# Performance work log

Measured on AMD Instinct MI355X. Metric: run time of the kernel, lower is better.

The kernel has to match this reference:

```python
import jax, jax.numpy as jnp
import numpy as np
import math

HIDDEN = 2048
NUM_HEADS = 32
NUM_KV_HEADS = 8
HEAD_DIM = HIDDEN // NUM_HEADS
GROUPS = NUM_HEADS // NUM_KV_HEADS
B, S = 2, 2048


def setup_inputs() -> dict:
    key = jax.random.key(0)
    ks = jax.random.split(key, 9)
    sc = 1.0 / math.sqrt(HIDDEN)
    x = jax.random.normal(ks[0], (B, S, HIDDEN), dtype=jnp.float32)
    # causal mask: 1 where attention allowed, 0 where masked
    mask = jnp.tril(jnp.ones((S, S), dtype=jnp.int32))[None, None, :, :]
    Wq = jax.random.normal(ks[1], (HIDDEN, HIDDEN), dtype=jnp.float32) * sc
    bq = jnp.zeros((HIDDEN,), dtype=jnp.float32)
    Wk = jax.random.normal(ks[2], (NUM_KV_HEADS * HEAD_DIM, HIDDEN), dtype=jnp.float32) * sc
    bk = jnp.zeros((NUM_KV_HEADS * HEAD_DIM,), dtype=jnp.float32)
    Wv = jax.random.normal(ks[3], (NUM_KV_HEADS * HEAD_DIM, HIDDEN), dtype=jnp.float32) * sc
    bv = jnp.zeros((NUM_KV_HEADS * HEAD_DIM,), dtype=jnp.float32)
    Wo = jax.random.normal(ks[4], (HIDDEN, HIDDEN), dtype=jnp.float32) * sc
    bo = jnp.zeros((HIDDEN,), dtype=jnp.float32)
    return {"x": x, "mask": mask, "Wq": Wq, "bq": bq, "Wk": Wk, "bk": bk,
            "Wv": Wv, "bv": bv, "Wo": Wo, "bo": bo}


def reference(x, mask, Wq, bq, Wk, bk, Wv, bv, Wo, bo):
    b, s, _ = x.shape
    # projections (torch Linear: y = x @ W.T + b)
    Q = (x @ Wq.T + bq).reshape(b, s, NUM_HEADS, HEAD_DIM).transpose(0, 2, 1, 3)  # b h s d
    K = (x @ Wk.T + bk).reshape(b, s, NUM_KV_HEADS, HEAD_DIM).transpose(0, 2, 1, 3)
    V = (x @ Wv.T + bv).reshape(b, s, NUM_KV_HEADS, HEAD_DIM).transpose(0, 2, 1, 3)
    # repeat_kv expansion
    K = jnp.repeat(K, GROUPS, axis=1)  # b h s d
    V = jnp.repeat(V, GROUPS, axis=1)
    scores = jnp.einsum('bhqd,bhkd->bhqk', Q, K) / math.sqrt(HEAD_DIM)
    scores = jnp.where(mask == 0, jnp.float32(-jnp.inf), scores)
    w = jax.nn.softmax(scores, axis=-1)
    # dropout is identity in eval mode
    out = jnp.einsum('bhqk,bhkd->bhqd', w, V)
    out = out.transpose(0, 2, 1, 3).reshape(b, s, HIDDEN)
    return out @ Wo.T + bo
```

## Files before the change

kernel.cpp:

```cpp
#include <hip/hip_runtime.h>
#include <hip/hip_bf16.h>
#include <stdint.h>

#define HID   2048
#define SLEN  2048
#define NB    2
#define NHEADS 32
#define NKVH   8
#define HDIM   64
#define KVW    512

typedef __bf16 bf16_t;
typedef __bf16 bf16x4 __attribute__((ext_vector_type(4)));
typedef __bf16 bf16x8 __attribute__((ext_vector_type(8)));
typedef float  f32x4  __attribute__((ext_vector_type(4)));

__device__ __forceinline__ f32x4 mfma16(bf16x8 a, bf16x8 b, f32x4 c) {
  return __builtin_amdgcn_mfma_f32_16x16x32_bf16(a, b, c, 0, 0, 0);
}

__device__ __forceinline__ void gl2lds16(const bf16_t* g, bf16_t* l) {
  __builtin_amdgcn_global_load_lds(
      (const __attribute__((address_space(1))) void*)g,
      (__attribute__((address_space(3))) void*)l,
      16, 0, 0);
}

__device__ __forceinline__ float fast_exp2(float x) {
#if __has_builtin(__builtin_amdgcn_exp2f)
  return __builtin_amdgcn_exp2f(x);
#else
  return __expf(x * 0.69314718f);
#endif
}

__device__ __forceinline__ bf16x8 ld8(const bf16_t* p) {
  return *(const bf16x8*)p;
}
__device__ __forceinline__ bf16x8 ld8(const float* p) {
  f32x4 a = *(const f32x4*)p;
  f32x4 b = *(const f32x4*)(p + 4);
  bf16x8 r;
  r[0] = (bf16_t)a[0]; r[1] = (bf16_t)a[1]; r[2] = (bf16_t)a[2]; r[3] = (bf16_t)a[3];
  r[4] = (bf16_t)b[0]; r[5] = (bf16_t)b[1]; r[6] = (bf16_t)b[2]; r[7] = (bf16_t)b[3];
  return r;
}

__device__ __forceinline__ void st_c(bf16_t* p, float v) { *p = (bf16_t)v; }
__device__ __forceinline__ void st_c(float*  p, float v) { *p = v; }

__global__ __launch_bounds__(256) void cvt_kernel(
    const float* __restrict__ x,  const float* __restrict__ wq,
    const float* __restrict__ wk, const float* __restrict__ wv,
    const float* __restrict__ wo,
    bf16_t* xb, bf16_t* wqb, bf16_t* wkb, bf16_t* wvb, bf16_t* wob)
{
  const float* s; bf16_t* d; size_t n;
  switch (blockIdx.y) {
    case 0:  s = x;  d = xb;  n = (size_t)NB * SLEN * HID; break;
    case 1:  s = wq; d = wqb; n = (size_t)HID * HID; break;
    case 2:  s = wk; d = wkb; n = (size_t)KVW * HID; break;
    case 3:  s = wv; d = wvb; n = (size_t)KVW * HID; break;
    default: s = wo; d = wob; n = (size_t)HID * HID; break;
  }
  const size_t stride = (size_t)gridDim.x * 256 * 8;
  for (size_t i = ((size_t)blockIdx.x * 256 + threadIdx.x) * 8; i < n; i += stride)
    *(bf16x8*)(d + i) = ld8(s + i);
}

template <typename CT, bool TRANSV>
__device__ __forceinline__ void gemm128_dma(
    const bf16_t* __restrict__ Ap, int lda,
    const bf16_t* __restrict__ Wp, int ldw,
    const float* __restrict__ biasp,
    CT* __restrict__ Cp, int ldc, int K,
    bf16_t* __restrict__ Al, bf16_t* __restrict__ Bl)
{
  const int tid  = threadIdx.x;
  const int lane = tid & 63;
  const int w    = tid >> 6;
  const int fr   = lane & 15;
  const int quad = lane >> 4;
  const int wm   = (w >> 1) * 64;
  const int wn   = (w & 1) * 64;

  const f32x4 z4 = {0.f, 0.f, 0.f, 0.f};
  f32x4 acc[4][4];
  for (int i = 0; i < 4; ++i)
    for (int j = 0; j < 4; ++j) acc[i][j] = z4;

  const int c0   = w * 4;
  const int srow = lane >> 2;
  const int skc  = (lane & 3) * 8;

  for (int k0 = 0; k0 < K; k0 += 64) {
    for (int t = 0; t < 4; ++t) {
      const int c  = c0 + t;
      const int r  = (c & 7) * 16 + srow;
      const int kk = k0 + (c >> 3) * 32 + skc;
      gl2lds16(Ap + (size_t)r * lda + kk, &Al[c * 512 + lane * 8]);
      gl2lds16(Wp + (size_t)r * ldw + kk, &Bl[c * 512 + lane * 8]);
    }
    __syncthreads();
    for (int ks = 0; ks < 2; ++ks) {
      bf16x8 af[4], bfr[4];
      for (int mi = 0; mi < 4; ++mi)
        af[mi] = *(const bf16x8*)&Al[ks * 4096 + (wm + mi * 16 + fr) * 32 + quad * 8];
      for (int ni = 0; ni < 4; ++ni)
        bfr[ni] = *(const bf16x8*)&Bl[ks * 4096 + (wn + ni * 16 + fr) * 32 + quad * 8];
      for (int mi = 0; mi < 4; ++mi)
        for (int ni = 0; ni < 4; ++ni)
          acc[mi][ni] = mfma16(af[mi], bfr[ni], acc[mi][ni]);
    }
    __syncthreads();
  }

  for (int ni = 0; ni < 4; ++ni) {
    const int col = wn + ni * 16 + fr;
    const float bz = biasp[col];
    for (int mi = 0; mi < 4; ++mi) {
      const int r0 = wm + mi * 16 + quad * 4;
      if constexpr (TRANSV) {
        bf16x4 pk;
        for (int r = 0; r < 4; ++r) pk[r] = (bf16_t)(acc[mi][ni][r] + bz);
        *(bf16x4*)&Cp[(size_t)col * ldc + r0] = pk;
      } else {
        for (int r = 0; r < 4; ++r)
          st_c(Cp + (size_t)(r0 + r) * ldc + col, acc[mi][ni][r] + bz);
      }
    }
  }
}

__global__ __launch_bounds__(256) void qkv_dma_kernel(
    const bf16_t* __restrict__ xb,
    const bf16_t* __restrict__ Wqb, const float* __restrict__ bq,
    const bf16_t* __restrict__ Wkb, const float* __restrict__ bk,
    const bf16_t* __restrict__ Wvb, const float* __restrict__ bv,
    bf16_t* Qb, bf16_t* Kb, bf16_t* VbT)
{
  __shared__ __align__(16) bf16_t Al[2 * 4096];
  __shared__ __align__(16) bf16_t Bl[2 * 4096];

  const int nb = blockIdx.x;
  const int mb = blockIdx.y;
  const bf16_t* A = xb + (size_t)mb * 128 * HID;
  if (nb < 16) {
    gemm128_dma<bf16_t, false>(A, HID, Wqb + (size_t)nb * 128 * HID, HID,
                               bq + nb * 128,
                               Qb + (size_t)mb * 128 * HID + nb * 128, HID, HID,
                               Al, Bl);
  } else if (nb < 20) {
    const int j = nb - 16;
    gemm128_dma<bf16_t, false>(A, HID, Wkb + (size_t)j * 128 * HID, HID,
                               bk + j * 128,
                               Kb + (size_t)mb * 128 * KVW + j * 128, KVW, HID,
                               Al, Bl);
  } else {
    const int j = nb - 20;
    const int b = mb >> 4;
    bf16_t* Cv = VbT + ((size_t)(b * NKVH + j * 2) * HDIM) * SLEN + (mb & 15) * 128;
    gemm128_dma<bf16_t, true>(A, HID, Wvb + (size_t)j * 128 * HID, HID,
                              bv + j * 128, Cv, SLEN, HID, Al, Bl);
  }
}

__global__ __launch_bounds__(256) void oproj_dma_kernel(
    const bf16_t* __restrict__ A, const bf16_t* __restrict__ Wob,
    const float* __restrict__ bo, float* out)
{
  __shared__ __align__(16) bf16_t Al[2 * 4096];
  __shared__ __align__(16) bf16_t Bl[2 * 4096];
  const int nb = blockIdx.x, mb = blockIdx.y;
  gemm128_dma<float, false>(A + (size_t)mb * 128 * HID, HID,
                            Wob + (size_t)nb * 128 * HID, HID,
                            bo + nb * 128,
                            out + (size_t)mb * 128 * HID + nb * 128, HID, HID,
                            Al, Bl);
}

template <typename AT, typename CT>
__device__ __forceinline__ void gemm128_tile(
    const AT* __restrict__ Ap, int lda,
    const float* __restrict__ Wp, int ldw,
    const float* __restrict__ biasp,
    CT* __restrict__ Cp, int ldc,
    int K)
{
  __shared__ __align__(16) bf16_t Al[128 * 32];
  __shared__ __align__(16) bf16_t Bl[128 * 32];

  const int tid  = threadIdx.x;
  const int lane = tid & 63;
  const int w    = tid >> 6;
  const int fr   = lane & 15;
  const int quad = lane >> 4;
  const int wm   = (w >> 1) * 64;
  const int wn   = (w & 1) * 64;

  const f32x4 z4 = {0.f, 0.f, 0.f, 0.f};
  f32x4 acc[4][4];
  for (int i = 0; i < 4; ++i)
    for (int j = 0; j < 4; ++j) acc[i][j] = z4;

  const int c0    = w * 2;
  const int srow0 = lane >> 2;
  const int skc   = (lane & 3) * 8;

  for (int k0 = 0; k0 < K; k0 += 32) {
    bf16x8 av[2], bv[2];
    for (int t = 0; t < 2; ++t) {
      const int r = (c0 + t) * 16 + srow0;
      av[t] = ld8(Ap + (size_t)r * lda + k0 + skc);
      bv[t] = ld8(Wp + (size_t)r * ldw + k0 + skc);
    }
    for (int t = 0; t < 2; ++t) {
      const int c = c0 + t;
      *(bf16x8*)&Al[c * 512 + lane * 8] = av[t];
      *(bf16x8*)&Bl[c * 512 + lane * 8] = bv[t];
    }
    __syncthreads();
    bf16x8 af[4], bfr[4];
    for (int mi = 0; mi < 4; ++mi)
      af[mi] = *(const bf16x8*)&Al[(wm + mi * 16 + fr) * 32 + quad * 8];
    for (int ni = 0; ni < 4; ++ni)
      bfr[ni] = *(const bf16x8*)&Bl[(wn + ni * 16 + fr) * 32 + quad * 8];
    for (int mi = 0; mi < 4; ++mi)
      for (int ni = 0; ni < 4; ++ni)
        acc[mi][ni] = mfma16(af[mi], bfr[ni], acc[mi][ni]);
    __syncthreads();
  }

  for (int ni = 0; ni < 4; ++ni) {
    const int col = wn + ni * 16 + fr;
    const float bz = biasp[col];
    for (int mi = 0; mi < 4; ++mi) {
      const int r0 = wm + mi * 16 + quad * 4;
      for (int r = 0; r < 4; ++r)
        st_c(Cp + (size_t)(r0 + r) * ldc + col, acc[mi][ni][r] + bz);
    }
  }
}

__global__ __launch_bounds__(256) void qkv_kernel(
    const float* __restrict__ x,
    const float* __restrict__ Wq, const float* __restrict__ bq,
    const float* __restrict__ Wk, const float* __restrict__ bk,
    const float* __restrict__ Wv, const float* __restrict__ bv,
    bf16_t* Qb, bf16_t* Kb, bf16_t* Vb)
{
  const int nb = blockIdx.x;
  const int mb = blockIdx.y;
  const float* W; const float* bias; bf16_t* C; int ldc;
  if (nb < 16)      { W = Wq + (size_t)nb * 128 * HID;  bias = bq + nb * 128;
                      C = Qb + nb * 128; ldc = HID; }
  else if (nb < 20) { const int j = nb - 16;
                      W = Wk + (size_t)j * 128 * HID;   bias = bk + j * 128;
                      C = Kb + j * 128; ldc = KVW; }
  else              { const int j = nb - 20;
                      W = Wv + (size_t)j * 128 * HID;   bias = bv + j * 128;
                      C = Vb + j * 128; ldc = KVW; }
  gemm128_tile<float, bf16_t>(x + (size_t)mb * 128 * HID, HID, W, HID, bias,
                              C + (size_t)mb * 128 * ldc, ldc, HID);
}

__global__ __launch_bounds__(256) void oproj_kernel(
    const bf16_t* __restrict__ A, const float* __restrict__ Wo,
    const float* __restrict__ bo, float* out)
{
  const int nb = blockIdx.x, mb = blockIdx.y;
  gemm128_tile<bf16_t, float>(A + (size_t)mb * 128 * HID, HID,
                              Wo + (size_t)nb * 128 * HID, HID,
                              bo + nb * 128,
                              out + (size_t)mb * 128 * HID + nb * 128, HID, HID);
}

__global__ __launch_bounds__(256) void vtrans_kernel(
    const bf16_t* __restrict__ Vb, bf16_t* __restrict__ VbT)
{
  __shared__ bf16_t T[64][72];
  const int st = blockIdx.x, kvh = blockIdx.y, b = blockIdx.z;
  const int tid = threadIdx.x;
  {
    const int row = tid >> 2;
    const int c16 = (tid & 3) * 16;
    const bf16_t* src =
        Vb + ((size_t)b * SLEN + st * 64 + row) * KVW + kvh * HDIM + c16;
    *(bf16x8*)&T[row][c16]     = *(const bf16x8*)(src);
    *(bf16x8*)&T[row][c16 + 8] = *(const bf16x8*)(src + 8);
  }
  __syncthreads();
  {
    const int d  = tid >> 2;
    const int sc = (tid & 3) * 16;
    bf16_t tmp[16];
    for (int j = 0; j < 16; ++j) tmp[j] = T[sc + j][d];
    bf16_t* dst = VbT + ((size_t)(b * NKVH + kvh) * HDIM + d) * SLEN + st * 64 + sc;
    *(bf16x8*)dst       = *(bf16x8*)&tmp[0];
    *(bf16x8*)(dst + 8) = *(bf16x8*)&tmp[8];
  }
}

__global__ __launch_bounds__(256) void attn_kernel(
    const bf16_t* Q, const bf16_t* __restrict__ Kg,
    const bf16_t* __restrict__ VT, bf16_t* O)
{
  const int pid = blockIdx.x;
  const int h   = blockIdx.y;
  const int b   = blockIdx.z;
  const int kvh = h >> 2;

  const int tid  = threadIdx.x;
  const int lane = tid & 63;
  const int w    = tid >> 6;
  const int fr   = lane & 15;
  const int quad = lane >> 4;

  const int PS  = 72;
  const int VTS = 136;
  __shared__ __align__(16) bf16_t KL[8192];
  __shared__ __align__(16) bf16_t PP[128 * 72];
  __shared__ __align__(16) bf16_t Vt[64 * 136];

  const size_t qbase = (size_t)b * SLEN;
  const bf16_t* VTh = VT + (size_t)(b * NKVH + kvh) * HDIM * SLEN;

  bf16x8 ones8;
  {
    const bf16_t o1 = (bf16_t)(fr == 0 ? 1.0f : 0.0f);
    for (int j = 0; j < 8; ++j) ones8[j] = o1;
  }

  for (int half = 0; half < 2; ++half) {
    const int qt = half ? (15 - pid) : pid;
    const int q0 = qt * 128;

    bf16x8 qf[2][2];
    for (int qi = 0; qi < 2; ++qi)
      for (int ks = 0; ks < 2; ++ks) {
        const size_t qrow = qbase + q0 + w * 32 + qi * 16 + fr;
        qf[qi][ks] = *(const bf16x8*)&Q[qrow * HID + h * HDIM + ks * 32 + quad * 8];
      }

    const f32x4 z4 = {0.f, 0.f, 0.f, 0.f};
    f32x4 o_acc[2][4];
    f32x4 o_l[2];
    for (int qi = 0; qi < 2; ++qi) {
      o_l[qi] = z4;
      for (int di = 0; di < 4; ++di) o_acc[qi][di] = z4;
    }

    for (int kt = 0; kt <= qt; ++kt) {
      const size_t krow0 = qbase + kt * 128;

      for (int t = 0; t < 4; ++t) {
        const int c  = w * 4 + t;
        const int hf = c >> 3;
        const int r  = (c & 7) * 16 + (lane >> 2);
        const int dk = hf * 32 + (lane & 3) * 8;
        gl2lds16(&Kg[(krow0 + r) * KVW + kvh * HDIM + dk], &KL[c * 512 + lane * 8]);
      }
      {
        const int d  = tid >> 2;
        const int kc = (tid & 3) * 32;
        const bf16_t* src = VTh + (size_t)d * SLEN + kt * 128 + kc;
        bf16x8 v0 = *(const bf16x8*)(src);
        bf16x8 v1 = *(const bf16x8*)(src + 8);
        bf16x8 v2 = *(const bf16x8*)(src + 16);
        bf16x8 v3 = *(const bf16x8*)(src + 24);
        bf16_t* dst = &Vt[d * VTS + kc];
        *(bf16x8*)(dst)      = v0;
        *(bf16x8*)(dst + 8)  = v1;
        *(bf16x8*)(dst + 16) = v2;
        *(bf16x8*)(dst + 24) = v3;
      }
      __syncthreads();

      f32x4 s[2][8];
      for (int qi = 0; qi < 2; ++qi)
        for (int ki = 0; ki < 8; ++ki) s[qi][ki] = z4;
      for (int ks = 0; ks < 2; ++ks)
        for (int ki = 0; ki < 8; ++ki) {
          bf16x8 kf = *(const bf16x8*)&KL[ks * 4096 + (ki * 16 + fr) * 32 + quad * 8];
          s[0][ki] = mfma16(qf[0][ks], kf, s[0][ki]);
          s[1][ki] = mfma16(qf[1][ks], kf, s[1][ki]);
        }

      const float C2 = 0.18033688f;
      const bool diag = (kt == qt);
      for (int hk = 0; hk < 2; ++hk) {
        for (int qi = 0; qi < 2; ++qi)
          for (int k2 = 0; k2 < 4; ++k2) {
            const int ki = hk * 4 + k2;
            for (int r = 0; r < 4; ++r) {
              float pe = fast_exp2(s[qi][ki][r] * C2);
              if (diag && (ki * 16 + fr > w * 32 + qi * 16 + quad * 4 + r))
                pe = 0.f;
              PP[(w * 32 + qi * 16 + quad * 4 + r) * PS + k2 * 16 + fr] =
                  (bf16_t)pe;
            }
          }
        for (int k2 = 0; k2 < 2; ++k2) {
          bf16x8 pf0 = *(const bf16x8*)&PP[(w * 32 + fr) * PS + k2 * 32 + quad * 8];
          bf16x8 pf1 = *(const bf16x8*)&PP[(w * 32 + 16 + fr) * PS + k2 * 32 + quad * 8];
          o_l[0] = mfma16(pf0, ones8, o_l[0]);
          o_l[1] = mfma16(pf1, ones8, o_l[1]);
          const int kb = hk * 64 + k2 * 32;
          for (int di = 0; di < 4; ++di) {
            bf16x8 vf = *(const bf16x8*)&Vt[(di * 16 + fr) * VTS + kb + quad * 8];
            o_acc[0][di] = mfma16(pf0, vf, o_acc[0][di]);
            o_acc[1][di] = mfma16(pf1, vf, o_acc[1][di]);
          }
        }
      }
      __syncthreads();
    }

    for (int qi = 0; qi < 2; ++qi)
      for (int r = 0; r < 4; ++r) {
        const float l  = __shfl(o_l[qi][r], lane & 48);
        const float rl = 1.f / l;
        const size_t qg_ = qbase + q0 + w * 32 + qi * 16 + quad * 4 + r;
        for (int di = 0; di < 4; ++di)
          O[qg_ * HID + h * HDIM + di * 16 + fr] = (bf16_t)(o_acc[qi][di][r] * rl);
      }
  }
}

extern "C" void kernel_launch(void* const* d_in, const int* in_sizes, int n_in,
                              void* d_out, int out_size, void* d_ws, size_t ws_size,
                              hipStream_t stream) {
  const float* x  = (const float*)d_in[0];
  const float* Wq = (const float*)d_in[2];
  const float* bq = (const float*)d_in[3];
  const float* Wk = (const float*)d_in[4];
  const float* bk = (const float*)d_in[5];
  const float* Wv = (const float*)d_in[6];
  const float* bv = (const float*)d_in[7];
  const float* Wo = (const float*)d_in[8];
  const float* bo = (const float*)d_in[9];
  float* out = (float*)d_out;

  const size_t M = (size_t)NB * SLEN;
  dim3 blk(256, 1, 1);

  const size_t needA = (M * HID
                        + (size_t)HID * HID
                        + (size_t)KVW * HID
                        + (size_t)KVW * HID
                        + (size_t)HID * HID
                        + M * HID
                        + M * KVW
                        + M * KVW) * 2;
  if (ws_size >= needA) {
    bf16_t* xb  = (bf16_t*)d_ws;
    bf16_t* Wqb = xb  + M * HID;
    bf16_t* Wkb = Wqb + (size_t)HID * HID;
    bf16_t* Wvb = Wkb + (size_t)KVW * HID;
    bf16_t* Wob = Wvb + (size_t)KVW * HID;
    bf16_t* Qb  = Wob + (size_t)HID * HID;
    bf16_t* Kb  = Qb  + M * HID;
    bf16_t* VbT = Kb  + M * KVW;

    cvt_kernel<<<dim3(1024, 5, 1), blk, 0, stream>>>(
        x, Wq, Wk, Wv, Wo, xb, Wqb, Wkb, Wvb, Wob);
    qkv_dma_kernel<<<dim3(24, 32, 1), blk, 0, stream>>>(
        xb, Wqb, bq, Wkb, bk, Wvb, bv, Qb, Kb, VbT);
    attn_kernel<<<dim3(8, 32, 2), blk, 0, stream>>>(Qb, Kb, VbT, Qb);
    oproj_dma_kernel<<<dim3(16, 32, 1), blk, 0, stream>>>(Qb, Wob, bo, out);
  } else {
    bf16_t* Qb  = (bf16_t*)d_ws;
    bf16_t* Kb  = Qb + M * HID;
    bf16_t* Vb  = Kb + M * KVW;
    bf16_t* VbT = Vb + M * KVW;

    qkv_kernel<<<dim3(24, 32, 1), blk, 0, stream>>>(x, Wq, bq, Wk, bk, Wv, bv, Qb, Kb, Vb);
    vtrans_kernel<<<dim3(32, 8, 2), blk, 0, stream>>>(Vb, VbT);
    attn_kernel<<<dim3(8, 32, 2), blk, 0, stream>>>(Qb, Kb, VbT, Qb);
    oproj_kernel<<<dim3(16, 32, 1), blk, 0, stream>>>(Qb, Wo, bo, out);
  }
}
```

Measured before the change: 325.0 us.

## Replace 128x128 projection GEMMs with double-buffered 256x256 8-wave pipelined GEMM

Replaces the QKV and output projection GEMMs with a 256x256-tile, 512-thread kernel that double-buffers LDS through global_load_lds, with XOR-swizzled LDS layout and interleaved prefetch/MFMA phases separated by barriers and s_setprio. The Q/K/V weight stacking is treated as one concatenated weight (Wq, Wk, Wv contiguous in the workspace) and the biases are copied into a concatenated buffer so a single grid covers all three projections. The goal is more data reuse per tile and overlap of global loads with MFMA work. The costs are far fewer blocks (192 and 128), which may underfill the GPU, plus 128KB of LDS per block and heavy register pressure.

```diff
diff --git a/kernel.cpp b/kernel.cpp
--- a/kernel.cpp
+++ b/kernel.cpp
@@ -68,115 +68,270 @@
     *(bf16x8*)(d + i) = ld8(s + i);
 }
 
-template <typename CT, bool TRANSV>
-__device__ __forceinline__ void gemm128_dma(
-    const bf16_t* __restrict__ Ap, int lda,
-    const bf16_t* __restrict__ Wp, int ldw,
-    const float* __restrict__ biasp,
-    CT* __restrict__ Cp, int ldc, int K,
-    bf16_t* __restrict__ Al, bf16_t* __restrict__ Bl)
+
+__device__ __forceinline__ bf16x8 ldfrag(const bf16_t* __restrict__ Lh, int r, int g) {
+  return *(const bf16x8*)(Lh + r * 64 + ((g ^ (r & 7)) << 3));
+}
+
+template <int Q>
+__device__ __forceinline__ void mfma_quad(const bf16x8 (&af)[2][2],
+                                          const bf16x8 (&bfr)[4][2],
+                                          f32x4 (&acc)[8][4]) {
+#pragma unroll
+  for (int ks = 0; ks < 2; ++ks)
+#pragma unroll
+    for (int i = 0; i < 2; ++i)
+#pragma unroll
+      for (int ni = 0; ni < 4; ++ni)
+        acc[2 * Q + i][ni] = mfma16(af[i][ks], bfr[ni][ks], acc[2 * Q + i][ni]);
+}
+
+__device__ __forceinline__ void phase_barrier() {
+  __builtin_amdgcn_s_barrier();
+  asm volatile("" ::: "memory");
+}
+
+__device__ __forceinline__ void gemm256_core(
+    const bf16_t* __restrict__ Ag,
+    const bf16_t* __restrict__ Bg,
+    bf16_t* __restrict__ lds, f32x4 (&acc)[8][4])
 {
   const int tid  = threadIdx.x;
   const int lane = tid & 63;
   const int w    = tid >> 6;
   const int fr   = lane & 15;
   const int quad = lane >> 4;
-  const int wm   = (w >> 1) * 64;
-  const int wn   = (w & 1) * 64;
+  const int wr   = w >> 2;
+  const int wc   = w & 3;
+  const int rbB  = (wc & 1) * 64;
+
+  bf16_t* A0 = lds;
+  bf16_t* B0 = lds + 16384;
+  bf16_t* A1 = lds + 32768;
+  bf16_t* B1 = lds + 49152;
+  const bf16_t* Ar0 = A0 + wr * 8192;
+  const bf16_t* Br0 = B0 + (wc >> 1) * 8192;
+  const bf16_t* Ar1 = A1 + wr * 8192;
+  const bf16_t* Br1 = B1 + (wc >> 1) * 8192;
 
   const f32x4 z4 = {0.f, 0.f, 0.f, 0.f};
-  f32x4 acc[4][4];
-  for (int i = 0; i < 4; ++i)
+#pragma unroll
+  for (int i = 0; i < 8; ++i)
+#pragma unroll
     for (int j = 0; j < 4; ++j) acc[i][j] = z4;
 
-  const int c0   = w * 4;
-  const int srow = lane >> 2;
-  const int skc  = (lane & 3) * 8;
-
-  for (int k0 = 0; k0 < K; k0 += 64) {
-    for (int t = 0; t < 4; ++t) {
-      const int c  = c0 + t;
-      const int r  = (c & 7) * 16 + srow;
-      const int kk = k0 + (c >> 3) * 32 + skc;
-      gl2lds16(Ap + (size_t)r * lda + kk, &Al[c * 512 + lane * 8]);
-      gl2lds16(Wp + (size_t)r * ldw + kk, &Bl[c * 512 + lane * 8]);
-    }
-    __syncthreads();
-    for (int ks = 0; ks < 2; ++ks) {
-      bf16x8 af[4], bfr[4];
-      for (int mi = 0; mi < 4; ++mi)
-        af[mi] = *(const bf16x8*)&Al[ks * 4096 + (wm + mi * 16 + fr) * 32 + quad * 8];
-      for (int ni = 0; ni < 4; ++ni)
-        bfr[ni] = *(const bf16x8*)&Bl[ks * 4096 + (wn + ni * 16 + fr) * 32 + quad * 8];
-      for (int mi = 0; mi < 4; ++mi)
-        for (int ni = 0; ni < 4; ++ni)
-          acc[mi][ni] = mfma16(af[mi], bfr[ni], acc[mi][ni]);
-    }
-    __syncthreads();
-  }
-
+  auto STAGE = [&](const bf16_t* __restrict__ Gp, bf16_t* __restrict__ Lh) {
+#pragma unroll
+    for (int j = 0; j < 2; ++j) {
+      const int s = j * 512 + tid;
+      const int r = s >> 3;
+      const int g = (s & 7) ^ (r & 7);
+      gl2lds16(Gp + (size_t)r * HID + g * 8, Lh + s * 8);
+    }
+  };
+
+  STAGE(Bg,                  B0);
+  STAGE(Bg + 128 * HID,      B0 + 8192);
+  STAGE(Ag,                  A0);
+  STAGE(Ag + 128 * HID,      A0 + 8192);
+  STAGE(Bg + 64,             B1);
+  STAGE(Bg + 128 * HID + 64, B1 + 8192);
+  asm volatile("s_waitcnt vmcnt(4)" ::: "memory");
+  phase_barrier();
+
+  bf16x8 bfr[4][2], af[2][2];
+
+#pragma unroll 1
+  for (int it = 0; it < 16; ++it) {
+    const bool more = (it < 15);
+    const size_t k1 = (size_t)(2 * it + 1) * 64;
+    const size_t k2 = (size_t)(2 * it + 2) * 64;
+    const size_t k3 = (size_t)(2 * it + 3) * 64;
+
+#pragma unroll
+    for (int ni = 0; ni < 4; ++ni)
+#pragma unroll
+      for (int ks = 0; ks < 2; ++ks)
+        bfr[ni][ks] = ldfrag(Br0, rbB + ni * 16 + fr, ks * 4 + quad);
+#pragma unroll
+    for (int i = 0; i < 2; ++i)
+#pragma unroll
+      for (int ks = 0; ks < 2; ++ks)
+        af[i][ks] = ldfrag(Ar0, i * 16 + fr, ks * 4 + quad);
+    STAGE(Ag + k1, A1);
+    phase_barrier();
+    asm volatile("s_waitcnt lgkmcnt(0)" ::: "memory");
+    __builtin_amdgcn_s_setprio(1);
+    mfma_quad<0>(af, bfr, acc);
+    __builtin_amdgcn_s_setprio(0);
+    phase_barrier();
+
+#pragma unroll
+    for (int i = 0; i < 2; ++i)
+#pragma unroll
+      for (int ks = 0; ks < 2; ++ks)
+        af[i][ks] = ldfrag(Ar0, 32 + i * 16 + fr, ks * 4 + quad);
+    STAGE(Ag + 128 * HID + k1, A1 + 8192);
+    phase_barrier();
+    asm volatile("s_waitcnt lgkmcnt(0)" ::: "memory");
+    __builtin_amdgcn_s_setprio(1);
+    mfma_quad<1>(af, bfr, acc);
+    __builtin_amdgcn_s_setprio(0);
+    phase_barrier();
+
+#pragma unroll
+    for (int i = 0; i < 2; ++i)
+#pragma unroll
+      for (int ks = 0; ks < 2; ++ks)
+        af[i][ks] = ldfrag(Ar0, 64 + i * 16 + fr, ks * 4 + quad);
+    if (more) STAGE(Bg + k2, B0);
+    phase_barrier();
+    asm volatile("s_waitcnt lgkmcnt(0)" ::: "memory");
+    __builtin_amdgcn_s_setprio(1);
+    mfma_quad<2>(af, bfr, acc);
+    __builtin_amdgcn_s_setprio(0);
+    phase_barrier();
+
+#pragma unroll
+    for (int i = 0; i < 2; ++i)
+#pragma unroll
+      for (int ks = 0; ks < 2; ++ks)
+        af[i][ks] = ldfrag(Ar0, 96 + i * 16 + fr, ks * 4 + quad);
+    if (more) STAGE(Bg + 128 * HID + k2, B0 + 8192);
+    phase_barrier();
+    asm volatile("s_waitcnt lgkmcnt(0)" ::: "memory");
+    __builtin_amdgcn_s_setprio(1);
+    mfma_quad<3>(af, bfr, acc);
+    __builtin_amdgcn_s_setprio(0);
+    if (more) { asm volatile("s_waitcnt vmcnt(4)" ::: "memory"); }
+    else      { asm volatile("s_waitcnt vmcnt(0)" ::: "memory"); }
+    phase_barrier();
+
+#pragma unroll
+    for (int ni = 0; ni < 4; ++ni)
+#pragma unroll
+      for (int ks = 0; ks < 2; ++ks)
+        bfr[ni][ks] = ldfrag(Br1, rbB + ni * 16 + fr, ks * 4 + quad);
+#pragma unroll
+    for (int i = 0; i < 2; ++i)
+#pragma unroll
+      for (int ks = 0; ks < 2; ++ks)
+        af[i][ks] = ldfrag(Ar1, i * 16 + fr, ks * 4 + quad);
+    if (more) STAGE(Ag + k2, A0);
+    phase_barrier();
+    asm volatile("s_waitcnt lgkmcnt(0)" ::: "memory");
+    __builtin_amdgcn_s_setprio(1);
+    mfma_quad<0>(af, bfr, acc);
+    __builtin_amdgcn_s_setprio(0);
+    phase_barrier();
+
+#pragma unroll
+    for (int i = 0; i < 2; ++i)
+#pragma unroll
+      for (int ks = 0; ks < 2; ++ks)
+        af[i][ks] = ldfrag(Ar1, 32 + i * 16 + fr, ks * 4 + quad);
+    if (more) STAGE(Ag + 128 * HID + k2, A0 + 8192);
+    phase_barrier();
+    asm volatile("s_waitcnt lgkmcnt(0)" ::: "memory");
+    __builtin_amdgcn_s_setprio(1);
+    mfma_quad<1>(af, bfr, acc);
+    __builtin_amdgcn_s_setprio(0);
+    phase_barrier();
+
+#pragma unroll
+    for (int i = 0; i < 2; ++i)
+#pragma unroll
+      for (int ks = 0; ks < 2; ++ks)
+        af[i][ks] = ldfrag(Ar1, 64 + i * 16 + fr, ks * 4 + quad);
+    if (more) STAGE(Bg + k3, B1);
+    phase_barrier();
+    asm volatile("s_waitcnt lgkmcnt(0)" ::: "memory");
+    __builtin_amdgcn_s_setprio(1);
+    mfma_quad<2>(af, bfr, acc);
+    __builtin_amdgcn_s_setprio(0);
+    phase_barrier();
+
+#pragma unroll
+    for (int i = 0; i < 2; ++i)
+#pragma unroll
+      for (int ks = 0; ks < 2; ++ks)
+        af[i][ks] = ldfrag(Ar1, 96 + i * 16 + fr, ks * 4 + quad);
+    if (more) STAGE(Bg + 128 * HID + k3, B1 + 8192);
+    phase_barrier();
+    asm volatile("s_waitcnt lgkmcnt(0)" ::: "memory");
+    __builtin_amdgcn_s_setprio(1);
+    mfma_quad<3>(af, bfr, acc);
+    __builtin_amdgcn_s_setprio(0);
+    if (more) { asm volatile("s_waitcnt vmcnt(4)" ::: "memory"); }
+    phase_barrier();
+  }
+}
+
+__global__ __launch_bounds__(512, 2) void qkv8_kernel(
+    const bf16_t* __restrict__ xb, const bf16_t* __restrict__ Wcat,
+    const float* __restrict__ bcat,
+    bf16_t* __restrict__ Qb, bf16_t* __restrict__ Kb, bf16_t* __restrict__ VbT)
+{
+  __shared__ __align__(16) bf16_t lds[65536];
+  const int cb = blockIdx.x;
+  const int mb = blockIdx.y;
+  f32x4 acc[8][4];
+  gemm256_core(xb + (size_t)mb * 256 * HID, Wcat + (size_t)cb * 256 * HID, lds, acc);
+
+  const int tid = threadIdx.x, lane = tid & 63, w = tid >> 6;
+  const int fr = lane & 15, quad = lane >> 4, wr = w >> 2, wc = w & 3;
+#pragma unroll
   for (int ni = 0; ni < 4; ++ni) {
-    const int col = wn + ni * 16 + fr;
-    const float bz = biasp[col];
-    for (int mi = 0; mi < 4; ++mi) {
-      const int r0 = wm + mi * 16 + quad * 4;
-      if constexpr (TRANSV) {
+    const int gcol = cb * 256 + wc * 64 + ni * 16 + fr;
+    const float bz = bcat[gcol];
+#pragma unroll
+    for (int mi = 0; mi < 8; ++mi) {
+      const int grow = mb * 256 + wr * 128 + mi * 16 + quad * 4;
+      if (cb < 8) {
+#pragma unroll
+        for (int r = 0; r < 4; ++r)
+          Qb[(size_t)(grow + r) * HID + gcol] = (bf16_t)(acc[mi][ni][r] + bz);
+      } else if (cb < 10) {
+        const int kc = gcol - 2048;
+#pragma unroll
+        for (int r = 0; r < 4; ++r)
+          Kb[(size_t)(grow + r) * KVW + kc] = (bf16_t)(acc[mi][ni][r] + bz);
+      } else {
+        const int vc = gcol - 2560;
+        const int b = grow >> 11, s = grow & 2047;
         bf16x4 pk;
+#pragma unroll
         for (int r = 0; r < 4; ++r) pk[r] = (bf16_t)(acc[mi][ni][r] + bz);
-        *(bf16x4*)&Cp[(size_t)col * ldc + r0] = pk;
-      } else {
-        for (int r = 0; r < 4; ++r)
-          st_c(Cp + (size_t)(r0 + r) * ldc + col, acc[mi][ni][r] + bz);
+        *(bf16x4*)&VbT[((size_t)(b * NKVH + (vc >> 6)) * HDIM + (vc & 63)) * SLEN + s] = pk;
       }
     }
   }
 }
 
-__global__ __launch_bounds__(256) void qkv_dma_kernel(
-    const bf16_t* __restrict__ xb,
-    const bf16_t* __restrict__ Wqb, const float* __restrict__ bq,
-    const bf16_t* __restrict__ Wkb, const float* __restrict__ bk,
-    const bf16_t* __restrict__ Wvb, const float* __restrict__ bv,
-    bf16_t* Qb, bf16_t* Kb, bf16_t* VbT)
-{
-  __shared__ __align__(16) bf16_t Al[2 * 4096];
-  __shared__ __align__(16) bf16_t Bl[2 * 4096];
-
-  const int nb = blockIdx.x;
+__global__ __launch_bounds__(512, 2) void oproj8_kernel(
+    const bf16_t* __restrict__ A, const bf16_t* __restrict__ Wob,
+    const float* __restrict__ bo, float* __restrict__ out)
+{
+  __shared__ __align__(16) bf16_t lds[65536];
+  const int cb = blockIdx.x;
   const int mb = blockIdx.y;
-  const bf16_t* A = xb + (size_t)mb * 128 * HID;
-  if (nb < 16) {
-    gemm128_dma<bf16_t, false>(A, HID, Wqb + (size_t)nb * 128 * HID, HID,
-                               bq + nb * 128,
-                               Qb + (size_t)mb * 128 * HID + nb * 128, HID, HID,
-                               Al, Bl);
-  } else if (nb < 20) {
-    const int j = nb - 16;
-    gemm128_dma<bf16_t, false>(A, HID, Wkb + (size_t)j * 128 * HID, HID,
-                               bk + j * 128,
-                               Kb + (size_t)mb * 128 * KVW + j * 128, KVW, HID,
-                               Al, Bl);
-  } else {
-    const int j = nb - 20;
-    const int b = mb >> 4;
-    bf16_t* Cv = VbT + ((size_t)(b * NKVH + j * 2) * HDIM) * SLEN + (mb & 15) * 128;
-    gemm128_dma<bf16_t, true>(A, HID, Wvb + (size_t)j * 128 * HID, HID,
-                              bv + j * 128, Cv, SLEN, HID, Al, Bl);
-  }
-}
-
-__global__ __launch_bounds__(256) void oproj_dma_kernel(
-    const bf16_t* __restrict__ A, const bf16_t* __restrict__ Wob,
-    const float* __restrict__ bo, float* out)
-{
-  __shared__ __align__(16) bf16_t Al[2 * 4096];
-  __shared__ __align__(16) bf16_t Bl[2 * 4096];
-  const int nb = blockIdx.x, mb = blockIdx.y;
-  gemm128_dma<float, false>(A + (size_t)mb * 128 * HID, HID,
-                            Wob + (size_t)nb * 128 * HID, HID,
-                            bo + nb * 128,
-                            out + (size_t)mb * 128 * HID + nb * 128, HID, HID,
-                            Al, Bl);
+  f32x4 acc[8][4];
+  gemm256_core(A + (size_t)mb * 256 * HID, Wob + (size_t)cb * 256 * HID, lds, acc);
+
+  const int tid = threadIdx.x, lane = tid & 63, w = tid >> 6;
+  const int fr = lane & 15, quad = lane >> 4, wr = w >> 2, wc = w & 3;
+#pragma unroll
+  for (int ni = 0; ni < 4; ++ni) {
+    const int gcol = cb * 256 + wc * 64 + ni * 16 + fr;
+    const float bz = bo[gcol];
+#pragma unroll
+    for (int mi = 0; mi < 8; ++mi) {
+      const int grow = mb * 256 + wr * 128 + mi * 16 + quad * 4;
+#pragma unroll
+      for (int r = 0; r < 4; ++r)
+        out[(size_t)(grow + r) * HID + gcol] = acc[mi][ni][r] + bz;
+    }
+  }
 }
 
 template <typename AT, typename CT>
@@ -451,7 +606,8 @@
                         + (size_t)HID * HID
                         + M * HID
                         + M * KVW
-                        + M * KVW) * 2;
+                        + M * KVW) * 2
+                       + (size_t)(HID + 2 * KVW) * sizeof(float);
   if (ws_size >= needA) {
     bf16_t* xb  = (bf16_t*)d_ws;
     bf16_t* Wqb = xb  + M * HID;
@@ -461,13 +617,21 @@
     bf16_t* Qb  = Wob + (size_t)HID * HID;
     bf16_t* Kb  = Qb  + M * HID;
     bf16_t* VbT = Kb  + M * KVW;
+    float*  bcat = (float*)(VbT + M * KVW);
 
     cvt_kernel<<<dim3(1024, 5, 1), blk, 0, stream>>>(
         x, Wq, Wk, Wv, Wo, xb, Wqb, Wkb, Wvb, Wob);
-    qkv_dma_kernel<<<dim3(24, 32, 1), blk, 0, stream>>>(
-        xb, Wqb, bq, Wkb, bk, Wvb, bv, Qb, Kb, VbT);
+    hipMemcpyAsync(bcat,             bq, HID * sizeof(float),
+                   hipMemcpyDeviceToDevice, stream);
+    hipMemcpyAsync(bcat + HID,       bk, KVW * sizeof(float),
+                   hipMemcpyDeviceToDevice, stream);
+    hipMemcpyAsync(bcat + HID + KVW, bv, KVW * sizeof(float),
+                   hipMemcpyDeviceToDevice, stream);
+    qkv8_kernel<<<dim3(12, 16, 1), dim3(512, 1, 1), 0, stream>>>(
+        xb, Wqb, bcat, Qb, Kb, VbT);
     attn_kernel<<<dim3(8, 32, 2), blk, 0, stream>>>(Qb, Kb, VbT, Qb);
-    oproj_dma_kernel<<<dim3(16, 32, 1), blk, 0, stream>>>(Qb, Wob, bo, out);
+    oproj8_kernel<<<dim3(8, 16, 1), dim3(512, 1, 1), 0, stream>>>(
+        Qb, Wob, bo, out);
   } else {
     bf16_t* Qb  = (bf16_t*)d_ws;
     bf16_t* Kb  = Qb + M * HID;
```

New measurement: 323.1 us. About the same (-0.6%).
